# Optimization experiments

Measured on AMD Instinct MI355X. Metric: run time of the kernel, lower is better.

The kernel has to match this reference:

```python
import jax, jax.numpy as jnp
import numpy as np

N, F, L, XN, YN = 500000, 8, 16, 8, 4

def setup_inputs() -> dict:
    key = jax.random.key(0)
    k1, k2, k3, k4, k5 = jax.random.split(key, 5)
    inp = jax.random.normal(k1, (N, F), dtype=jnp.float32)
    x = jax.random.normal(k2, (N, XN), dtype=jnp.float32)
    c = jax.random.normal(k3, (F, L), dtype=jnp.float32)
    # widths in [0.5, 1.5) to avoid exp underflow / div-by-tiny
    b = jax.random.uniform(k4, (F, L), dtype=jnp.float32) + 0.5
    w = jax.random.normal(k5, (L, XN, YN), dtype=jnp.float32)
    return {"inp": inp, "x": x, "c": c, "b": b, "w": w}

def reference(inp, x, c, b, w):
    # Gaussian membership: mu[n, f, l] = exp(-(inp[n,f] - c[f,l])^2 / (2 b[f,l]^2))
    d = inp[:, :, None] - c[None, :, :]                      # [N, F, L]
    mu = jnp.exp(-(d * d) / (2.0 * b * b)[None, :, :])       # [N, F, L]
    # Rule firing strength: product over features, + 0.001 (as in torch code)
    firing = jnp.prod(mu, axis=1) + 0.001                    # [N, L]
    # Normalize over rules
    norm = firing / jnp.sum(firing, axis=1, keepdims=True)   # [N, L]
    # Per-rule linear consequents: rule_out[n, l, y] = x[n] @ w[l]
    rule_out = jnp.einsum('nx,lxy->nly', x, w)               # [N, L, YN]
    # Weighted combine over rules
    out = jnp.einsum('nl,nly->ny', norm, rule_out)           # [N, YN]
    # Match torch output layouts: disanceng [L, N], diwuceng [YN, N]
    return (norm.T, out.T)
```

## Files before the change

kernel.cpp:

```cpp
#include <hip/hip_runtime.h>

#define F 8
#define L 16
#define XN 8
#define YN 4

__global__ __launch_bounds__(256) void eafnn_kernel(
    const float* __restrict__ inp,
    const float* __restrict__ x,
    const float* __restrict__ c,
    const float* __restrict__ b,
    const float* __restrict__ w,
    float* __restrict__ out,
    int n_total)
{
    __shared__ __attribute__((aligned(16))) float s_c[F * L];
    __shared__ __attribute__((aligned(16))) float s_k[F * L];
    __shared__ __attribute__((aligned(16))) float s_w[L * XN * YN];

    const int tid = threadIdx.x;
    if (tid < F * L) {
        float bb = b[tid];
        s_c[tid] = c[tid];
        s_k[tid] = -1.4426950408889634f / (2.0f * bb * bb);
    }
    for (int i = tid; i < L * XN * YN; i += 256) s_w[i] = w[i];
    __syncthreads();

    const int n = blockIdx.x * 256 + tid;
    if (n >= n_total) return;

    const float4* ip = (const float4*)(inp + (size_t)n * F);
    float4 a0 = ip[0], a1 = ip[1];
    float fi[F] = {a0.x, a0.y, a0.z, a0.w, a1.x, a1.y, a1.z, a1.w};

    float s[L];
#pragma unroll
    for (int l = 0; l < L; ++l) s[l] = 0.0f;

#pragma unroll
    for (int f = 0; f < F; ++f) {
        float v = fi[f];
#pragma unroll
        for (int lq = 0; lq < L / 4; ++lq) {
            float4 cq = *(const float4*)&s_c[f * L + lq * 4];
            float4 kq = *(const float4*)&s_k[f * L + lq * 4];
            float d0 = v - cq.x, d1 = v - cq.y, d2 = v - cq.z, d3 = v - cq.w;
            s[lq * 4 + 0] = fmaf(d0 * d0, kq.x, s[lq * 4 + 0]);
            s[lq * 4 + 1] = fmaf(d1 * d1, kq.y, s[lq * 4 + 1]);
            s[lq * 4 + 2] = fmaf(d2 * d2, kq.z, s[lq * 4 + 2]);
            s[lq * 4 + 3] = fmaf(d3 * d3, kq.w, s[lq * 4 + 3]);
        }
    }

    float firing[L];
    float tot = 0.0f;
#pragma unroll
    for (int l = 0; l < L; ++l) {
        firing[l] = __builtin_amdgcn_exp2f(s[l]) + 0.001f;
        tot += firing[l];
    }
    float inv = 1.0f / tot;

    float norm[L];
#pragma unroll
    for (int l = 0; l < L; ++l) {
        norm[l] = firing[l] * inv;
        out[(size_t)l * n_total + n] = norm[l];
    }

    const float4* xp = (const float4*)(x + (size_t)n * XN);
    float4 x0 = xp[0], x1 = xp[1];
    float xv[XN] = {x0.x, x0.y, x0.z, x0.w, x1.x, x1.y, x1.z, x1.w};

    float weff[XN * YN];
#pragma unroll
    for (int i = 0; i < XN * YN; ++i) weff[i] = 0.0f;

#pragma unroll
    for (int l = 0; l < L; ++l) {
        float nl = norm[l];
#pragma unroll
        for (int i = 0; i < XN * YN; i += 4) {
            float4 wq = *(const float4*)&s_w[l * XN * YN + i];
            weff[i + 0] = fmaf(nl, wq.x, weff[i + 0]);
            weff[i + 1] = fmaf(nl, wq.y, weff[i + 1]);
            weff[i + 2] = fmaf(nl, wq.z, weff[i + 2]);
            weff[i + 3] = fmaf(nl, wq.w, weff[i + 3]);
        }
    }

    float acc[YN] = {0.f, 0.f, 0.f, 0.f};
#pragma unroll
    for (int xx = 0; xx < XN; ++xx) {
#pragma unroll
        for (int y = 0; y < YN; ++y)
            acc[y] = fmaf(xv[xx], weff[xx * YN + y], acc[y]);
    }

    float* out_y = out + (size_t)L * n_total;
#pragma unroll
    for (int y = 0; y < YN; ++y)
        out_y[(size_t)y * n_total + n] = acc[y];
}

extern "C" void kernel_launch(void* const* d_in, const int* in_sizes, int n_in,
                              void* d_out, int out_size, void* d_ws, size_t ws_size,
                              hipStream_t stream) {
    const float* inp = (const float*)d_in[0];
    const float* x   = (const float*)d_in[1];
    const float* c   = (const float*)d_in[2];
    const float* b   = (const float*)d_in[3];
    const float* w   = (const float*)d_in[4];
    float* out = (float*)d_out;

    int n_total = in_sizes[0] / F;
    int grid = (n_total + 255) / 256;
    eafnn_kernel<<<grid, 256, 0, stream>>>(inp, x, c, b, w, out, n_total);
}
```

Baseline: 24.10 us.

## Expand Gaussian exponent to polynomial and read weights from global uniformly

Expands the squared distance k*(v-c)^2 into A*v^2 + B*v + C, with per-rule constants summed once into C0. This turns the exponent accumulation into two FMAs per term and removes the subtract and multiply. The weight matrix is no longer staged in shared memory; it is read with uniform global loads, and the consequent is computed per rule as x@w[l] then weighted. Loads of x are hoisted early, and out-of-range threads are clamped instead of returning early. The expanded form can lose precision through cancellation when inputs are far from the centres.

```diff
diff --git a/kernel.cpp b/kernel.cpp
--- a/kernel.cpp
+++ b/kernel.cpp
@@ -4,6 +4,7 @@
 #define L 16
 #define XN 8
 #define YN 4
+#define BLK 256
 
 __global__ __launch_bounds__(256) void eafnn_kernel(
     const float* __restrict__ inp,
@@ -14,94 +15,106 @@
     float* __restrict__ out,
     int n_total)
 {
-    __shared__ __attribute__((aligned(16))) float s_c[F * L];
-    __shared__ __attribute__((aligned(16))) float s_k[F * L];
-    __shared__ __attribute__((aligned(16))) float s_w[L * XN * YN];
+    __shared__ __attribute__((aligned(16))) float s_A[F * L];
+    __shared__ __attribute__((aligned(16))) float s_B[F * L];
+    __shared__ __attribute__((aligned(16))) float s_Cp[F * L];
+    __shared__ __attribute__((aligned(16))) float s_C0[L];
 
     const int tid = threadIdx.x;
     if (tid < F * L) {
-        float bb = b[tid];
-        s_c[tid] = c[tid];
-        s_k[tid] = -1.4426950408889634f / (2.0f * bb * bb);
+        float bb = b[tid], cc = c[tid];
+        float k = -1.4426950408889634f / (2.0f * bb * bb);
+        s_A[tid] = k;
+        s_B[tid] = -2.0f * k * cc;
+        s_Cp[tid] = k * cc * cc;
     }
-    for (int i = tid; i < L * XN * YN; i += 256) s_w[i] = w[i];
+    __syncthreads();
+    if (tid < L) {
+        float a = 0.0f;
+#pragma unroll
+        for (int f = 0; f < F; ++f) a += s_Cp[f * L + tid];
+        s_C0[tid] = a;
+    }
     __syncthreads();
 
-    const int n = blockIdx.x * 256 + tid;
-    if (n >= n_total) return;
+    int n = blockIdx.x * BLK + tid;
+    const bool ok = (n < n_total);
+    if (!ok) n = n_total - 1;
 
     const float4* ip = (const float4*)(inp + (size_t)n * F);
     float4 a0 = ip[0], a1 = ip[1];
     float fi[F] = {a0.x, a0.y, a0.z, a0.w, a1.x, a1.y, a1.z, a1.w};
 
-    float s[L];
+    const float4* xp = (const float4*)(x + (size_t)n * XN);
+    float4 x0 = xp[0], x1 = xp[1];
+    float xv[XN] = {x0.x, x0.y, x0.z, x0.w, x1.x, x1.y, x1.z, x1.w};
+
+    float sacc[L];
 #pragma unroll
-    for (int l = 0; l < L; ++l) s[l] = 0.0f;
+    for (int lq = 0; lq < L / 4; ++lq) {
+        float4 cq = *(const float4*)&s_C0[lq * 4];
+        sacc[lq * 4 + 0] = cq.x;
+        sacc[lq * 4 + 1] = cq.y;
+        sacc[lq * 4 + 2] = cq.z;
+        sacc[lq * 4 + 3] = cq.w;
+    }
 
 #pragma unroll
     for (int f = 0; f < F; ++f) {
         float v = fi[f];
+        float v2 = v * v;
 #pragma unroll
         for (int lq = 0; lq < L / 4; ++lq) {
-            float4 cq = *(const float4*)&s_c[f * L + lq * 4];
-            float4 kq = *(const float4*)&s_k[f * L + lq * 4];
-            float d0 = v - cq.x, d1 = v - cq.y, d2 = v - cq.z, d3 = v - cq.w;
-            s[lq * 4 + 0] = fmaf(d0 * d0, kq.x, s[lq * 4 + 0]);
-            s[lq * 4 + 1] = fmaf(d1 * d1, kq.y, s[lq * 4 + 1]);
-            s[lq * 4 + 2] = fmaf(d2 * d2, kq.z, s[lq * 4 + 2]);
-            s[lq * 4 + 3] = fmaf(d3 * d3, kq.w, s[lq * 4 + 3]);
+            float4 Aq = *(const float4*)&s_A[f * L + lq * 4];
+            float4 Bq = *(const float4*)&s_B[f * L + lq * 4];
+            sacc[lq * 4 + 0] = fmaf(Aq.x, v2, fmaf(Bq.x, v, sacc[lq * 4 + 0]));
+            sacc[lq * 4 + 1] = fmaf(Aq.y, v2, fmaf(Bq.y, v, sacc[lq * 4 + 1]));
+            sacc[lq * 4 + 2] = fmaf(Aq.z, v2, fmaf(Bq.z, v, sacc[lq * 4 + 2]));
+            sacc[lq * 4 + 3] = fmaf(Aq.w, v2, fmaf(Bq.w, v, sacc[lq * 4 + 3]));
         }
     }
 
-    float firing[L];
     float tot = 0.0f;
 #pragma unroll
     for (int l = 0; l < L; ++l) {
-        firing[l] = __builtin_amdgcn_exp2f(s[l]) + 0.001f;
-        tot += firing[l];
+        float fr = __builtin_amdgcn_exp2f(sacc[l]) + 0.001f;
+        sacc[l] = fr;
+        tot += fr;
     }
     float inv = 1.0f / tot;
-
-    float norm[L];
 #pragma unroll
     for (int l = 0; l < L; ++l) {
-        norm[l] = firing[l] * inv;
-        out[(size_t)l * n_total + n] = norm[l];
-    }
-
-    const float4* xp = (const float4*)(x + (size_t)n * XN);
-    float4 x0 = xp[0], x1 = xp[1];
-    float xv[XN] = {x0.x, x0.y, x0.z, x0.w, x1.x, x1.y, x1.z, x1.w};
-
-    float weff[XN * YN];
-#pragma unroll
-    for (int i = 0; i < XN * YN; ++i) weff[i] = 0.0f;
-
-#pragma unroll
-    for (int l = 0; l < L; ++l) {
-        float nl = norm[l];
-#pragma unroll
-        for (int i = 0; i < XN * YN; i += 4) {
-            float4 wq = *(const float4*)&s_w[l * XN * YN + i];
-            weff[i + 0] = fmaf(nl, wq.x, weff[i + 0]);
-            weff[i + 1] = fmaf(nl, wq.y, weff[i + 1]);
-            weff[i + 2] = fmaf(nl, wq.z, weff[i + 2]);
-            weff[i + 3] = fmaf(nl, wq.w, weff[i + 3]);
-        }
+        float nl = sacc[l] * inv;
+        sacc[l] = nl;
+        if (ok) out[(size_t)l * n_total + n] = nl;
     }
 
     float acc[YN] = {0.f, 0.f, 0.f, 0.f};
 #pragma unroll
-    for (int xx = 0; xx < XN; ++xx) {
+    for (int l = 0; l < L; ++l) {
+        float t0 = 0.f, t1 = 0.f, t2 = 0.f, t3 = 0.f;
 #pragma unroll
-        for (int y = 0; y < YN; ++y)
-            acc[y] = fmaf(xv[xx], weff[xx * YN + y], acc[y]);
+        for (int i = 0; i < XN; ++i) {
+            float4 wq = *(const float4*)&w[(l * XN + i) * YN];
+            float xs = xv[i];
+            t0 = fmaf(xs, wq.x, t0);
+            t1 = fmaf(xs, wq.y, t1);
+            t2 = fmaf(xs, wq.z, t2);
+            t3 = fmaf(xs, wq.w, t3);
+        }
+        float nl = sacc[l];
+        acc[0] = fmaf(nl, t0, acc[0]);
+        acc[1] = fmaf(nl, t1, acc[1]);
+        acc[2] = fmaf(nl, t2, acc[2]);
+        acc[3] = fmaf(nl, t3, acc[3]);
     }
 
     float* out_y = out + (size_t)L * n_total;
+    if (ok) {
 #pragma unroll
-    for (int y = 0; y < YN; ++y)
-        out_y[(size_t)y * n_total + n] = acc[y];
+        for (int y = 0; y < YN; ++y)
+            out_y[(size_t)y * n_total + n] = acc[y];
+    }
 }
 
 extern "C" void kernel_launch(void* const* d_in, const int* in_sizes, int n_in,
@@ -115,6 +128,6 @@
     float* out = (float*)d_out;
 
     int n_total = in_sizes[0] / F;
-    int grid = (n_total + 255) / 256;
-    eafnn_kernel<<<grid, 256, 0, stream>>>(inp, x, c, b, w, out, n_total);
+    int grid = (n_total + BLK - 1) / BLK;
+    eafnn_kernel<<<grid, BLK, 0, stream>>>(inp, x, c, b, w, out, n_total);
 }
```

After: 22.28 us. 1.08x faster.
